# Performance work log

Measured on AMD Instinct MI355X. Metric: run time of the kernel, lower is better.

Reference implementation:

```python
import jax, jax.numpy as jnp
import numpy as np

NUM_HEADS = 8

def _ln(x, w, b, eps=1e-5):
    m = x.mean(-1, keepdims=True)
    v = ((x - m) ** 2).mean(-1, keepdims=True)
    return (x - m) / jnp.sqrt(v + eps) * w + b

def _conv3(x, w, b):
    y = jax.lax.conv_general_dilated(x, w, (1, 1), 'SAME',
                                     dimension_numbers=('NCHW', 'OIHW', 'NCHW'))
    return y + b[None, :, None, None]

def _pos_encoding(c, h, w, dtype):
    # first c//2 channels: x position in [0,1]; next c//2: y position
    px = jnp.broadcast_to(jnp.linspace(0, 1, w, dtype=dtype)[None, :], (h, w))
    py = jnp.broadcast_to(jnp.linspace(0, 1, h, dtype=dtype)[:, None], (h, w))
    pe = jnp.concatenate([jnp.broadcast_to(px, (c // 2, h, w)),
                          jnp.broadcast_to(py, (c // 2, h, w))], axis=0)
    return pe[None]  # [1,c,h,w]

def _pixel_shuffle(x, r=2):
    b, c4, h, w = x.shape
    c = c4 // (r * r)
    return x.reshape(b, c, r, r, h, w).transpose(0, 1, 4, 2, 5, 3).reshape(b, c, h * r, w * r)

def _forward(x, text_hidden, proj_w, proj_b, cf_w, cf_b,
             blk_qw, blk_qb, blk_kw, blk_kb, blk_vw, blk_vb,
             blk_ow, blk_ob, blk_ln1w, blk_ln1b, blk_ln2w, blk_ln2b,
             up_w, up_b, cl_w, cl_b):
    B = x.shape[0]
    # text projection: [B, L, text_dim] -> [B, L, C]
    tf = jnp.einsum('bld,cd->blc', text_hidden, proj_w) + proj_b
    feat = _conv3(x, cf_w, cf_b)  # [B, C, H, W]
    _, C, H, W = feat.shape
    L = tf.shape[1]
    hd = C // NUM_HEADS
    scale = hd ** (-0.5)
    pe = _pos_encoding(C, H, W, feat.dtype)

    def block(feat, p):
        qw, qb, kw, kb, vw, vb, ow, ob, l1w, l1b, l2w, l2b = p
        q = jnp.einsum('oi,bihw->bohw', qw, feat) + qb[None, :, None, None]
        q = q + pe * 0.05
        q_flat = q.reshape(B, C, H * W).transpose(0, 2, 1)  # [B, HW, C]
        q_norm = _ln(q_flat, l1w, l1b)
        qh = q_norm.reshape(B, H * W, NUM_HEADS, hd).transpose(0, 2, 1, 3)
        k = jnp.einsum('blc,oc->blo', tf, kw) + kb
        v = jnp.einsum('blc,oc->blo', tf, vw) + vb
        kn = _ln(k, l2w, l2b)
        kh = kn.reshape(B, L, NUM_HEADS, hd).transpose(0, 2, 1, 3)
        vh = v.reshape(B, L, NUM_HEADS, hd).transpose(0, 2, 1, 3)
        attn = jax.nn.softmax(jnp.einsum('bhnd,bhld->bhnl', qh, kh) * scale, axis=-1)
        out = jnp.einsum('bhnl,bhld->bhnd', attn, vh)          # [B, H8, HW, hd]
        out = out.transpose(0, 2, 1, 3).reshape(B, H * W, C)   # [B, HW, C]
        out = out.transpose(0, 2, 1).reshape(B, C, H, W)
        out = jnp.einsum('oi,bihw->bohw', ow, out) + ob[None, :, None, None]
        return out + feat, None

    blk_params = (blk_qw, blk_qb, blk_kw, blk_kb, blk_vw, blk_vb,
                  blk_ow, blk_ob, blk_ln1w, blk_ln1b, blk_ln2w, blk_ln2b)
    feat, _ = jax.lax.scan(block, feat, blk_params)

    for i in range(up_w.shape[0]):
        feat = jax.nn.relu(_pixel_shuffle(_conv3(feat, up_w[i], up_b[i]), 2))
    return _conv3(feat, cl_w, cl_b)


def setup_inputs() -> dict:
    key = jax.random.key(0)
    ks = jax.random.split(key, 20)
    B, H, W = 8, 64, 64
    C, D, L, NB = 64, 512, 77, 16
    s = 0.05
    inp = {
        'x': jax.random.normal(ks[0], (B, 3, H, W), jnp.float32),
        'text_hidden': jax.random.normal(ks[1], (B, L, D), jnp.float32),
        'proj_w': jax.random.normal(ks[2], (C, D), jnp.float32) * 0.01,
        'proj_b': jnp.zeros((C,), jnp.float32),
        'cf_w': jax.random.normal(ks[3], (C, 3, 3, 3), jnp.float32) * s,
        'cf_b': jnp.zeros((C,), jnp.float32),
        'blk_qw': jax.random.normal(ks[4], (NB, C, C), jnp.float32) * s,
        'blk_qb': jnp.zeros((NB, C), jnp.float32),
        'blk_kw': jax.random.normal(ks[5], (NB, C, C), jnp.float32) * 0.01,
        'blk_kb': jnp.zeros((NB, C), jnp.float32),
        'blk_vw': jax.random.normal(ks[6], (NB, C, C), jnp.float32) * 0.01,
        'blk_vb': jnp.zeros((NB, C), jnp.float32),
        'blk_ow': jax.random.normal(ks[7], (NB, C, C), jnp.float32) * s,
        'blk_ob': jnp.zeros((NB, C), jnp.float32),
        'blk_ln1w': jnp.ones((NB, C), jnp.float32),
        'blk_ln1b': jnp.zeros((NB, C), jnp.float32),
        'blk_ln2w': jnp.ones((NB, C), jnp.float32),
        'blk_ln2b': jnp.zeros((NB, C), jnp.float32),
        'up_w': jax.random.normal(ks[8], (2, C * 4, C, 3, 3), jnp.float32) * s,
        'up_b': jnp.zeros((2, C * 4), jnp.float32),
        'cl_w': jax.random.normal(ks[9], (3, C, 3, 3), jnp.float32) * s,
        'cl_b': jnp.zeros((3,), jnp.float32),
    }
    return inp


def reference(x, text_hidden, proj_w, proj_b, cf_w, cf_b,
              blk_qw, blk_qb, blk_kw, blk_kb, blk_vw, blk_vb,
              blk_ow, blk_ob, blk_ln1w, blk_ln1b, blk_ln2w, blk_ln2b,
              up_w, up_b, cl_w, cl_b):
    return _forward(x, text_hidden, proj_w, proj_b, cf_w, cf_b,
                    blk_qw, blk_qb, blk_kw, blk_kb, blk_vw, blk_vb,
                    blk_ow, blk_ob, blk_ln1w, blk_ln1b, blk_ln2w, blk_ln2b,
                    up_w, up_b, cl_w, cl_b)
```

## Files before the change

### kernel.cpp

```cpp
#include <hip/hip_runtime.h>
#include <math.h>

#define BATCH 8
#define C 64
#define NH 8
#define HD 8
#define LTXT 77
#define H0 64
#define W0 64
#define HW0 (H0*W0)

typedef __attribute__((ext_vector_type(8))) short bfrag;
typedef __attribute__((ext_vector_type(4))) float ffrag;
typedef __attribute__((ext_vector_type(8))) unsigned short us8;
typedef __attribute__((ext_vector_type(4))) unsigned short us4;
typedef __attribute__((ext_vector_type(2))) float f2;

__device__ __forceinline__ unsigned short f2bf(float f) {
    unsigned u = __builtin_bit_cast(unsigned, f);
    u += 0x7fff + ((u >> 16) & 1);
    return (unsigned short)(u >> 16);
}

__global__ void text_proj_kernel(const float* __restrict__ th, const float* __restrict__ pw,
                                 const float* __restrict__ pb, float* __restrict__ tf) {
    __shared__ float sh[512];
    int bl = blockIdx.x;
    int c = threadIdx.x;
    const float* row = th + (size_t)bl * 512;
    for (int i = c; i < 512; i += 64) sh[i] = row[i];
    __syncthreads();
    const float* wrow = pw + c * 512;
    float acc = pb[c];
    for (int i = 0; i < 512; i += 4) {
        acc += sh[i] * wrow[i] + sh[i+1] * wrow[i+1] + sh[i+2] * wrow[i+2] + sh[i+3] * wrow[i+3];
    }
    tf[bl * 64 + c] = acc;
}

__global__ void __launch_bounds__(256)
prep_kernel(const float* __restrict__ x, const float* __restrict__ cf_w,
            const float* __restrict__ cf_b, float* __restrict__ feat,
            const float* __restrict__ up_w,
            unsigned short* __restrict__ PW1, unsigned short* __restrict__ PW2,
            const float* __restrict__ cl_w, unsigned short* __restrict__ PWF,
            const float* __restrict__ qw, const float* __restrict__ ow,
            unsigned short* __restrict__ PQ, unsigned short* __restrict__ PO) {
    int blk = blockIdx.x;
    if (blk < 8192) {
        int idx = blk * 256 + threadIdx.x;
        int wx = idx & 63;
        int h = (idx >> 6) & 63;
        int o = (idx >> 12) & 63;
        int b = idx >> 18;
        const float* wr = cf_w + o * 27;
        float acc = cf_b[o];
        for (int ci = 0; ci < 3; ci++) {
            for (int ky = 0; ky < 3; ky++) {
                int y = h + ky - 1;
                if ((unsigned)y >= 64u) continue;
                const float* xr = x + (((size_t)b * 3 + ci) * 64 + y) * 64;
                const float* wk = wr + ci * 9 + ky * 3;
                if (wx > 0) acc += xr[wx - 1] * wk[0];
                acc += xr[wx] * wk[1];
                if (wx < 63) acc += xr[wx + 1] * wk[2];
            }
        }
        feat[idx] = acc;
    } else if (blk < 8192 + 1152) {
        int e0 = blk - 8192;
        int st = e0 / 576;
        int e = (e0 % 576) * 256 + threadIdx.x;
        const float* w = up_w + (size_t)st * 147456;
        unsigned short* d = st ? PW2 : PW1;
        int j = e & 7, n = (e >> 3) & 255, q = (e >> 11) & 3, s = (e >> 13) & 1, t = e >> 14;
        int c = n & 63, g = n >> 6;
        int co = 4 * c + g, ci = 32 * s + 8 * q + j;
        d[e] = f2bf(w[co * 576 + ci * 9 + t]);
    } else if (blk < 8192 + 1152 + 36) {
        int e = (blk - 8192 - 1152) * 256 + threadIdx.x;
        int j = e & 7, n = (e >> 3) & 15, q = (e >> 7) & 3, s = (e >> 9) & 1, t = e >> 10;
        int ci = 32 * s + 8 * q + j;
        float v = (n < 3) ? cl_w[n * 576 + ci * 9 + t] : 0.f;
        PWF[e] = f2bf(v);
    } else {
        int e = (blk - 8192 - 1152 - 36) * 256 + threadIdx.x;
        int j = e & 7, n = (e >> 3) & 63, quad = (e >> 9) & 3, kt = (e >> 11) & 1, layer = e >> 12;
        int c = kt * 32 + quad * 8 + j;
        PQ[e] = f2bf(qw[layer * 4096 + n * 64 + c]);
        PO[e] = f2bf(ow[layer * 4096 + n * 64 + c]);
    }
}

__global__ void kv_all_kernel(const float* __restrict__ tf,
                              const float* __restrict__ kw, const float* __restrict__ kb,
                              const float* __restrict__ vw, const float* __restrict__ vb,
                              const float* __restrict__ l2w, const float* __restrict__ l2b,
                              float* __restrict__ kbuf, float* __restrict__ vbuf) {
    __shared__ float sh[64];
    int g = blockIdx.x;
    int bl = g % (BATCH * LTXT);
    int blk = g / (BATCH * LTXT);
    int o = threadIdx.x;
    sh[o] = tf[bl * 64 + o];
    __syncthreads();
    const float* kr = kw + blk * 4096 + o * 64;
    const float* vr = vw + blk * 4096 + o * 64;
    float ka = kb[blk * 64 + o], va = vb[blk * 64 + o];
    for (int c2 = 0; c2 < 64; c2++) {
        float t = sh[c2];
        ka += t * kr[c2];
        va += t * vr[c2];
    }
    float s = ka;
    for (int off = 32; off; off >>= 1) s += __shfl_xor(s, off, 64);
    float mean = s * (1.0f / 64.0f);
    float d = ka - mean;
    float s2 = d * d;
    for (int off = 32; off; off >>= 1) s2 += __shfl_xor(s2, off, 64);
    float rstd = rsqrtf(s2 * (1.0f / 64.0f) + 1e-5f);
    size_t outi = (size_t)blk * (BATCH * LTXT * 64) + (size_t)bl * 64 + o;
    kbuf[outi] = (d * rstd * l2w[blk * 64 + o] + l2b[blk * 64 + o]) * 0.51006973f;
    vbuf[outi] = va;
}

__global__ void __launch_bounds__(1024, 8)
attn_all_kernel(const float* __restrict__ feat,
                const float* __restrict__ kbuf, const float* __restrict__ vbuf,
                const unsigned short* __restrict__ PQ, const unsigned short* __restrict__ PO,
                const float* __restrict__ qb_a, const float* __restrict__ ob_a,
                const float* __restrict__ l1w_a, const float* __restrict__ l1b_a,
                unsigned short* __restrict__ X1) {
    __shared__ __attribute__((aligned(16))) unsigned short sfb[64][72];
    __shared__ __attribute__((aligned(16))) unsigned short sob[64][72];
    __shared__ __attribute__((aligned(16))) float qf[64][68];
    __shared__ float so[64][64];
    __shared__ __attribute__((aligned(16))) float red[2][4][64];
    __shared__ float ss1[8][64];

    int b = blockIdx.x >> 6;
    int tile = blockIdx.x & 63;
    int n0 = tile << 6;
    int wv = __builtin_amdgcn_readfirstlane(threadIdx.x >> 6);
    int lane = threadIdx.x & 63;
    int p = lane;
    int quad = lane >> 4, n16 = lane & 15;
    int mt = wv >> 2, nt = wv & 3;
    int o0 = wv * 4;
    int h = wv >> 1, half = wv & 1;
    int a0 = h * 8;
    const float* fbase = feat + ((size_t)b << 18) + n0;

    float rres[4];
#pragma unroll
    for (int j = 0; j < 4; j++) rres[j] = fbase[(o0 + j) * HW0 + p];
    {
        us4 v;
#pragma unroll
        for (int j = 0; j < 4; j++) v[j] = f2bf(rres[j]);
        *(us4*)&sfb[p][o0] = v;
    }

    const float pxk = 0.05f / 63.0f;
    float py005 = (float)tile * pxk;
    __syncthreads();

#pragma unroll 1
    for (int layer = 0; layer < 16; layer++) {
        const float* qb = qb_a + layer * 64;
        const float* ob = ob_a + layer * 64;
        const float* l1w = l1w_a + layer * 64;
        const float* l1b = l1b_a + layer * 64;

        {
            bfrag af0 = *(const bfrag*)&sfb[mt * 16 + n16][quad * 8];
            bfrag af1 = *(const bfrag*)&sfb[mt * 16 + n16][32 + quad * 8];
            const unsigned short* bq = PQ + layer * 4096 + (size_t)((quad * 64) + nt * 16 + n16) * 8;
            bfrag bf0 = *(const bfrag*)bq;
            bfrag bf1 = *(const bfrag*)(bq + 2048);
            ffrag cc = (ffrag)0.f;
            cc = __builtin_amdgcn_mfma_f32_16x16x32_bf16(af0, bf0, cc, 0, 0, 0);
            cc = __builtin_amdgcn_mfma_f32_16x16x32_bf16(af1, bf1, cc, 0, 0, 0);
            int cch = nt * 16 + n16;
            float qbv = qb[cch];
            int p0 = mt * 16 + quad * 4;
            float pe0 = (nt < 2) ? (float)p0 * pxk : py005;
            float ped = (nt < 2) ? pxk : 0.f;
            float ov[4];
            ov[0] = cc[0] + qbv + pe0;
            ov[1] = cc[1] + qbv + pe0 + ped;
            ov[2] = cc[2] + qbv + pe0 + 2.f * ped;
            ov[3] = cc[3] + qbv + pe0 + 3.f * ped;
            float4 o4 = {ov[0], ov[1], ov[2], ov[3]};
            *(float4*)&qf[cch][p0] = o4;

            float sv[4], sq[4];
#pragma unroll
            for (int r = 0; r < 4; r++) {
                float s = ov[r], s2v = ov[r] * ov[r];
                s += __shfl_xor(s, 1);  s2v += __shfl_xor(s2v, 1);
                s += __shfl_xor(s, 2);  s2v += __shfl_xor(s2v, 2);
                s += __shfl_xor(s, 4);  s2v += __shfl_xor(s2v, 4);
                s += __shfl_xor(s, 8);  s2v += __shfl_xor(s2v, 8);
                sv[r] = s; sq[r] = s2v;
            }
            if (n16 == 0) {
                *(float4*)&red[0][nt][p0] = (float4){sv[0], sv[1], sv[2], sv[3]};
                *(float4*)&red[1][nt][p0] = (float4){sq[0], sq[1], sq[2], sq[3]};
            }
        }
        __syncthreads();

        {
            float ts = red[0][0][p] + red[0][1][p] + red[0][2][p] + red[0][3][p];
            float ts2 = red[1][0][p] + red[1][1][p] + red[1][2][p] + red[1][3][p];
            float mean = ts * (1.0f / 64.0f);
            float var = ts2 * (1.0f / 64.0f) - mean * mean;
            float rstd = rsqrtf(var + 1e-5f);

            f2 qv[4];
#pragma unroll
            for (int j = 0; j < 4; j++) {
                float qa  = (qf[a0 + 2 * j][p]     - mean) * rstd * l1w[a0 + 2 * j]     + l1b[a0 + 2 * j];
                float qbv = (qf[a0 + 2 * j + 1][p] - mean) * rstd * l1w[a0 + 2 * j + 1] + l1b[a0 + 2 * j + 1];
                qv[j][0] = qa;
                qv[j][1] = qbv;
            }
            const float* kb_b = kbuf + ((size_t)layer * BATCH * LTXT + (size_t)b * LTXT) * 64 + a0;
            const float* vb_b = vbuf + ((size_t)layer * BATCH * LTXT + (size_t)b * LTXT) * 64 + a0;
            int l0 = half ? 39 : 0;
            int l1 = half ? 77 : 39;
            float ssum = 0.f;
            f2 acc2[4] = {(f2)0.f, (f2)0.f, (f2)0.f, (f2)0.f};
            for (int l = l0; l < l1; l++) {
                const float4* kr = (const float4*)(kb_b + l * 64);
                float4 k0 = kr[0], k1 = kr[1];
                f2 d2 = qv[0] * (f2){k0.x, k0.y};
                d2 += qv[1] * (f2){k0.z, k0.w};
                d2 += qv[2] * (f2){k1.x, k1.y};
                d2 += qv[3] * (f2){k1.z, k1.w};
                float e = exp2f(d2[0] + d2[1]);
                ssum += e;
                const float4* vr = (const float4*)(vb_b + l * 64);
                float4 v0 = vr[0], v1 = vr[1];
                f2 e2 = {e, e};
                acc2[0] += e2 * (f2){v0.x, v0.y};
                acc2[1] += e2 * (f2){v0.z, v0.w};
                acc2[2] += e2 * (f2){v1.x, v1.y};
                acc2[3] += e2 * (f2){v1.z, v1.w};
            }
            if (half) {
#pragma unroll
                for (int j = 0; j < 4; j++) {
                    so[a0 + 2 * j][p] = acc2[j][0];
                    so[a0 + 2 * j + 1][p] = acc2[j][1];
                }
                ss1[h][p] = ssum;
            }
            __syncthreads();
            if (!half) {
                float inv = 1.0f / (ssum + ss1[h][p]);
                us8 v;
#pragma unroll
                for (int j = 0; j < 4; j++) {
                    v[2*j]   = f2bf((acc2[j][0] + so[a0 + 2*j][p]) * inv);
                    v[2*j+1] = f2bf((acc2[j][1] + so[a0 + 2*j+1][p]) * inv);
                }
                *(us8*)&sob[p][a0] = v;
            }
        }
        __syncthreads();

        {
            bfrag af0 = *(const bfrag*)&sob[mt * 16 + n16][quad * 8];
            bfrag af1 = *(const bfrag*)&sob[mt * 16 + n16][32 + quad * 8];
            const unsigned short* bo = PO + layer * 4096 + (size_t)((quad * 64) + nt * 16 + n16) * 8;
            bfrag bf0 = *(const bfrag*)bo;
            bfrag bf1 = *(const bfrag*)(bo + 2048);
            ffrag cc = (ffrag)0.f;
            cc = __builtin_amdgcn_mfma_f32_16x16x32_bf16(af0, bf0, cc, 0, 0, 0);
            cc = __builtin_amdgcn_mfma_f32_16x16x32_bf16(af1, bf1, cc, 0, 0, 0);
            int cch = nt * 16 + n16;
            float obv = ob[cch];
            int p0 = mt * 16 + quad * 4;
            float4 o4;
            o4.x = cc[0] + obv; o4.y = cc[1] + obv; o4.z = cc[2] + obv; o4.w = cc[3] + obv;
            *(float4*)&qf[cch][p0] = o4;
        }
        __syncthreads();

        {
            us4 v;
#pragma unroll
            for (int j = 0; j < 4; j++) {
                rres[j] += qf[o0 + j][p];
                v[j] = f2bf(rres[j]);
            }
            *(us4*)&sfb[p][o0] = v;
        }
        __syncthreads();
    }

    us4 v;
#pragma unroll
    for (int j = 0; j < 4; j++) v[j] = f2bf(rres[j]);
    *(us4*)(X1 + ((size_t)(b * 4096 + n0 + p)) * 64 + o0) = v;
}

__global__ void __launch_bounds__(256)
upconv_mfma_kernel(const unsigned short* __restrict__ X, const unsigned short* __restrict__ Bp,
                   const float* __restrict__ bias, unsigned short* __restrict__ Y,
                   int Hin, int Win) {
    __shared__ __attribute__((aligned(16))) unsigned short sx[3 * 66 * 72];

    int y = blockIdx.y;
    int wv = threadIdx.x >> 6;
    int lane = threadIdx.x & 63;
    int q = lane >> 4, n16 = lane & 15;
    int m0 = blockIdx.x * 64;
    int hw = Hin * Win;
    int b = m0 / hw, rem = m0 % hw;
    int h = rem / Win, w0 = rem % Win;
    const unsigned short* Xb = X + (size_t)b * hw * 64;

    const us8 z8 = (us8)(unsigned short)0;
    for (int e = threadIdx.x; e < 1584; e += 256) {
        int ch8 = e & 7;
        int pxi = (e >> 3) % 66;
        int row = e / 528;
        int hh = h + row - 1, wp = w0 + pxi - 1;
        us8 v = z8;
        if ((unsigned)hh < (unsigned)Hin && (unsigned)wp < (unsigned)Win)
            v = *(const us8*)(Xb + ((size_t)hh * Win + wp) * 64 + ch8 * 8);
        *(us8*)&sx[row * 4752 + pxi * 72 + ch8 * 8] = v;
    }
    __syncthreads();

    ffrag acc[4][2];
#pragma unroll
    for (int i = 0; i < 4; i++)
#pragma unroll
        for (int j2 = 0; j2 < 2; j2++) acc[i][j2] = (ffrag)0.f;

    int npb = y * 128 + wv * 32;

    for (int t = 0; t < 9; t++) {
        int dy = t / 3, dx = t % 3;
        bfrag af[4][2];
#pragma unroll
        for (int mt = 0; mt < 4; mt++) {
            const unsigned short* sp = &sx[dy * 4752 + (mt * 16 + n16 + dx) * 72 + q * 8];
            af[mt][0] = *(const bfrag*)sp;
            af[mt][1] = *(const bfrag*)(sp + 32);
        }
#pragma unroll
        for (int s = 0; s < 2; s++) {
#pragma unroll
            for (int nt = 0; nt < 2; nt++) {
                bfrag bf = *(const bfrag*)(Bp + (size_t)((((t * 2 + s) * 4 + q) * 256) + npb + nt * 16 + n16) * 8);
#pragma unroll
                for (int mt = 0; mt < 4; mt++)
                    acc[mt][nt] = __builtin_amdgcn_mfma_f32_16x16x32_bf16(af[mt][s], bf, acc[mt][nt], 0, 0, 0);
            }
        }
    }

    int g = y * 2 + (wv >> 1);
    int r1 = y, r2 = wv >> 1;
    int cbase = (wv & 1) * 32;
    float bv[2];
#pragma unroll
    for (int nt = 0; nt < 2; nt++) bv[nt] = bias[4 * (cbase + nt * 16 + n16) + g];
    int Wo = Win * 2;
    unsigned short* Yb = Y + ((size_t)b * Hin * 2 * Wo + (size_t)(2 * h + r1) * Wo + r2) * 64;
#pragma unroll
    for (int mt = 0; mt < 4; mt++) {
#pragma unroll
        for (int r = 0; r < 4; r++) {
            int m = mt * 16 + q * 4 + r;
            unsigned short* dst = Yb + (size_t)(2 * (w0 + m)) * 64;
#pragma unroll
            for (int nt = 0; nt < 2; nt++) {
                float v = acc[mt][nt][r] + bv[nt];
                v = fmaxf(v, 0.f);
                dst[cbase + nt * 16 + n16] = f2bf(v);
            }
        }
    }
}

__global__ void __launch_bounds__(256)
final_mfma_kernel(const unsigned short* __restrict__ X, const unsigned short* __restrict__ Bp,
                  const float* __restrict__ bias, float* __restrict__ out) {
    __shared__ __attribute__((aligned(16))) unsigned short sx[6 * 66 * 72];

    int t0 = blockIdx.x;
    int wseg = t0 & 3;
    int rg = (t0 >> 2) & 63;
    int b = t0 >> 8;
    int y0 = rg * 4, w0 = wseg * 64;
    int wv = threadIdx.x >> 6, lane = threadIdx.x & 63;
    int q = lane >> 4, n16 = lane & 15;
    const unsigned short* Xb = X + (size_t)b * 65536 * 64;

    const us8 z8 = (us8)(unsigned short)0;
    for (int e = threadIdx.x; e < 3168; e += 256) {
        int ch8 = e & 7;
        int pxi = (e >> 3) % 66;
        int row = e / 528;
        int hh = y0 - 1 + row, wp = w0 - 1 + pxi;
        us8 v = z8;
        if ((unsigned)hh < 256u && (unsigned)wp < 256u)
            v = *(const us8*)(Xb + ((size_t)hh * 256 + wp) * 64 + ch8 * 8);
        *(us8*)&sx[row * 4752 + pxi * 72 + ch8 * 8] = v;
    }
    __syncthreads();

    ffrag acc[4];
#pragma unroll
    for (int i = 0; i < 4; i++) acc[i] = (ffrag)0.f;

    for (int t = 0; t < 9; t++) {
        int dy = t / 3, dx = t % 3;
        bfrag af[4][2];
#pragma unroll
        for (int mt = 0; mt < 4; mt++) {
            const unsigned short* sp = &sx[(wv + dy) * 4752 + (mt * 16 + n16 + dx) * 72 + q * 8];
            af[mt][0] = *(const bfrag*)sp;
            af[mt][1] = *(const bfrag*)(sp + 32);
        }
#pragma unroll
        for (int s = 0; s < 2; s++) {
            bfrag bf = *(const bfrag*)(Bp + (size_t)((((t * 2 + s) * 4 + q) * 16) + n16) * 8);
#pragma unroll
            for (int mt = 0; mt < 4; mt++)
                acc[mt] = __builtin_amdgcn_mfma_f32_16x16x32_bf16(af[mt][s], bf, acc[mt], 0, 0, 0);
        }
    }

    if (n16 < 3) {
        float bj = bias[n16];
        float* ob = out + (((size_t)b * 3 + n16) * 256 + (y0 + wv)) * 256;
#pragma unroll
        for (int mt = 0; mt < 4; mt++)
#pragma unroll
            for (int r = 0; r < 4; r++)
                ob[w0 + mt * 16 + q * 4 + r] = acc[mt][r] + bj;
    }
}

extern "C" void kernel_launch(void* const* d_in, const int* in_sizes, int n_in,
                              void* d_out, int out_size, void* d_ws, size_t ws_size,
                              hipStream_t stream) {
    const float* x      = (const float*)d_in[0];
    const float* th     = (const float*)d_in[1];
    const float* proj_w = (const float*)d_in[2];
    const float* proj_b = (const float*)d_in[3];
    const float* cf_w   = (const float*)d_in[4];
    const float* cf_b   = (const float*)d_in[5];
    const float* qw     = (const float*)d_in[6];
    const float* qb     = (const float*)d_in[7];
    const float* kw     = (const float*)d_in[8];
    const float* kb     = (const float*)d_in[9];
    const float* vw     = (const float*)d_in[10];
    const float* vb     = (const float*)d_in[11];
    const float* ow     = (const float*)d_in[12];
    const float* ob     = (const float*)d_in[13];
    const float* l1w    = (const float*)d_in[14];
    const float* l1b    = (const float*)d_in[15];
    const float* l2w    = (const float*)d_in[16];
    const float* l2b    = (const float*)d_in[17];
    const float* up_w   = (const float*)d_in[18];
    const float* up_b   = (const float*)d_in[19];
    const float* cl_w   = (const float*)d_in[20];
    const float* cl_b   = (const float*)d_in[21];

    float* ws   = (float*)d_ws;
    float* feat = ws;
    float* tf   = feat + 2097152;
    float* kbuf = tf + 39424;
    float* vbuf = kbuf + 630784;
    unsigned short* X1  = (unsigned short*)(vbuf + 630784);
    unsigned short* X2  = X1 + 2097152;
    unsigned short* X3  = X2 + 8388608;
    unsigned short* PW1 = X3 + 33554432;
    unsigned short* PW2 = PW1 + 147456;
    unsigned short* PWF = PW2 + 147456;
    unsigned short* PQ  = PWF + 9216;
    unsigned short* PO  = PQ + 65536;

    hipLaunchKernelGGL(prep_kernel, dim3(8192 + 1152 + 36 + 256), dim3(256), 0, stream,
                       x, cf_w, cf_b, feat, up_w, PW1, PW2, cl_w, PWF, qw, ow, PQ, PO);
    hipLaunchKernelGGL(text_proj_kernel, dim3(BATCH * LTXT), dim3(64), 0, stream,
                       th, proj_w, proj_b, tf);
    hipLaunchKernelGGL(kv_all_kernel, dim3(16 * BATCH * LTXT), dim3(64), 0, stream,
                       tf, kw, kb, vw, vb, l2w, l2b, kbuf, vbuf);

    hipLaunchKernelGGL(attn_all_kernel, dim3(BATCH * (HW0 / 64)), dim3(1024), 0, stream,
                       feat, kbuf, vbuf, PQ, PO, qb, ob, l1w, l1b, X1);

    hipLaunchKernelGGL(upconv_mfma_kernel, dim3(BATCH * 64 * 64 / 64, 2), dim3(256), 0, stream,
                       X1, PW1, up_b, X2, 64, 64);
    hipLaunchKernelGGL(upconv_mfma_kernel, dim3(BATCH * 128 * 128 / 64, 2), dim3(256), 0, stream,
                       X2, PW2, up_b + 256, X3, 128, 128);
    hipLaunchKernelGGL(final_mfma_kernel, dim3(BATCH * 64 * 4), dim3(256), 0, stream,
                       X3, PWF, cl_b, (float*)d_out);
}
```

Measured before the change: 583.1 us.

## Compute cross-attention scores and PV with bf16 MFMA instead of scalar FP32 loops

Moves the per-pixel attention over the 77 text tokens from scalar FP32 dot products to bf16 MFMA instructions, for both QK^T and P·V. The K/V producer now writes bf16 K padded to 80 rows and a transposed, padded V for MFMA-friendly loads. Q is normalized straight into a bf16 LDS tile, and the exp probabilities are staged in LDS as bf16, reusing a shared pool with qf. This trades FP32 accuracy in scores and probabilities for bf16, and adds four passes per layer, each with its own barriers, plus lanes that sit idle on padded MFMA tiles.

```diff
diff --git a/kernel.cpp b/kernel.cpp
--- a/kernel.cpp
+++ b/kernel.cpp
@@ -14,7 +14,6 @@
 typedef __attribute__((ext_vector_type(4))) float ffrag;
 typedef __attribute__((ext_vector_type(8))) unsigned short us8;
 typedef __attribute__((ext_vector_type(4))) unsigned short us4;
-typedef __attribute__((ext_vector_type(2))) float f2;
 
 __device__ __forceinline__ unsigned short f2bf(float f) {
     unsigned u = __builtin_bit_cast(unsigned, f);
@@ -96,21 +95,28 @@
                               const float* __restrict__ kw, const float* __restrict__ kb,
                               const float* __restrict__ vw, const float* __restrict__ vb,
                               const float* __restrict__ l2w, const float* __restrict__ l2b,
-                              float* __restrict__ kbuf, float* __restrict__ vbuf) {
+                              unsigned short* __restrict__ k16, unsigned short* __restrict__ vt16) {
     __shared__ float sh[64];
     int g = blockIdx.x;
-    int bl = g % (BATCH * LTXT);
-    int blk = g / (BATCH * LTXT);
+    int t = g % 96;
+    int lb = g / 96;
+    int b = lb & 7;
+    int blk = lb >> 3;
     int o = threadIdx.x;
-    sh[o] = tf[bl * 64 + o];
+    if (t >= LTXT) {
+        if (t < 80) k16[((size_t)lb * 80 + t) * 64 + o] = 0;
+        vt16[((size_t)lb * 64 + o) * 96 + t] = 0;
+        return;
+    }
+    sh[o] = tf[(b * LTXT + t) * 64 + o];
     __syncthreads();
-    const float* kr = kw + blk * 4096 + o * 64;
-    const float* vr = vw + blk * 4096 + o * 64;
+    const float* krw = kw + blk * 4096 + o * 64;
+    const float* vrw = vw + blk * 4096 + o * 64;
     float ka = kb[blk * 64 + o], va = vb[blk * 64 + o];
     for (int c2 = 0; c2 < 64; c2++) {
-        float t = sh[c2];
-        ka += t * kr[c2];
-        va += t * vr[c2];
+        float tv = sh[c2];
+        ka += tv * krw[c2];
+        va += tv * vrw[c2];
     }
     float s = ka;
     for (int off = 32; off; off >>= 1) s += __shfl_xor(s, off, 64);
@@ -119,24 +125,27 @@
     float s2 = d * d;
     for (int off = 32; off; off >>= 1) s2 += __shfl_xor(s2, off, 64);
     float rstd = rsqrtf(s2 * (1.0f / 64.0f) + 1e-5f);
-    size_t outi = (size_t)blk * (BATCH * LTXT * 64) + (size_t)bl * 64 + o;
-    kbuf[outi] = (d * rstd * l2w[blk * 64 + o] + l2b[blk * 64 + o]) * 0.51006973f;
-    vbuf[outi] = va;
+    float kn = (d * rstd * l2w[blk * 64 + o] + l2b[blk * 64 + o]) * 0.51006973f;
+    k16[((size_t)lb * 80 + t) * 64 + o] = f2bf(kn);
+    vt16[((size_t)lb * 64 + o) * 96 + t] = f2bf(va);
 }
 
 __global__ void __launch_bounds__(1024, 8)
 attn_all_kernel(const float* __restrict__ feat,
-                const float* __restrict__ kbuf, const float* __restrict__ vbuf,
+                const unsigned short* __restrict__ k16, const unsigned short* __restrict__ vt16,
                 const unsigned short* __restrict__ PQ, const unsigned short* __restrict__ PO,
                 const float* __restrict__ qb_a, const float* __restrict__ ob_a,
                 const float* __restrict__ l1w_a, const float* __restrict__ l1b_a,
                 unsigned short* __restrict__ X1) {
     __shared__ __attribute__((aligned(16))) unsigned short sfb[64][72];
     __shared__ __attribute__((aligned(16))) unsigned short sob[64][72];
-    __shared__ __attribute__((aligned(16))) float qf[64][68];
-    __shared__ float so[64][64];
+    __shared__ __attribute__((aligned(16))) unsigned short qn[64][72];
     __shared__ __attribute__((aligned(16))) float red[2][4][64];
-    __shared__ float ss1[8][64];
+    __shared__ float dpart[2][8][16];
+    __shared__ __attribute__((aligned(16))) char upool[2 * 64 * 104 * 2];
+
+    unsigned short (*P16)[64][104] = (unsigned short (*)[64][104])upool;
+    float (*qf)[68] = (float (*)[68])upool;
 
     int b = blockIdx.x >> 6;
     int tile = blockIdx.x & 63;
@@ -147,8 +156,10 @@
     int quad = lane >> 4, n16 = lane & 15;
     int mt = wv >> 2, nt = wv & 3;
     int o0 = wv * 4;
-    int h = wv >> 1, half = wv & 1;
-    int a0 = h * 8;
+    int cch = nt * 16 + n16;
+    int p0 = mt * 16 + quad * 4;
+    int h1 = wv >> 3, ntp = (wv >> 1) & 3, ms = wv & 1;
+    int pxl = ntp * 16 + n16;
     const float* fbase = feat + ((size_t)b << 18) + n0;
 
     float rres[4];
@@ -163,6 +174,7 @@
 
     const float pxk = 0.05f / 63.0f;
     float py005 = (float)tile * pxk;
+    const bfrag zb = (bfrag)(short)0;
     __syncthreads();
 
 #pragma unroll 1
@@ -171,28 +183,25 @@
         const float* ob = ob_a + layer * 64;
         const float* l1w = l1w_a + layer * 64;
         const float* l1b = l1b_a + layer * 64;
-
+        size_t kvbase = (size_t)layer * BATCH + b;
+
+        float ov[4];
         {
             bfrag af0 = *(const bfrag*)&sfb[mt * 16 + n16][quad * 8];
             bfrag af1 = *(const bfrag*)&sfb[mt * 16 + n16][32 + quad * 8];
-            const unsigned short* bq = PQ + layer * 4096 + (size_t)((quad * 64) + nt * 16 + n16) * 8;
-            bfrag bf0 = *(const bfrag*)bq;
-            bfrag bf1 = *(const bfrag*)(bq + 2048);
+            const unsigned short* bqp = PQ + layer * 4096 + (size_t)((quad * 64) + nt * 16 + n16) * 8;
+            bfrag bf0 = *(const bfrag*)bqp;
+            bfrag bf1 = *(const bfrag*)(bqp + 2048);
             ffrag cc = (ffrag)0.f;
             cc = __builtin_amdgcn_mfma_f32_16x16x32_bf16(af0, bf0, cc, 0, 0, 0);
             cc = __builtin_amdgcn_mfma_f32_16x16x32_bf16(af1, bf1, cc, 0, 0, 0);
-            int cch = nt * 16 + n16;
             float qbv = qb[cch];
-            int p0 = mt * 16 + quad * 4;
             float pe0 = (nt < 2) ? (float)p0 * pxk : py005;
             float ped = (nt < 2) ? pxk : 0.f;
-            float ov[4];
             ov[0] = cc[0] + qbv + pe0;
             ov[1] = cc[1] + qbv + pe0 + ped;
             ov[2] = cc[2] + qbv + pe0 + 2.f * ped;
             ov[3] = cc[3] + qbv + pe0 + 3.f * ped;
-            float4 o4 = {ov[0], ov[1], ov[2], ov[3]};
-            *(float4*)&qf[cch][p0] = o4;
 
             float sv[4], sq[4];
 #pragma unroll
@@ -212,64 +221,84 @@
         __syncthreads();
 
         {
-            float ts = red[0][0][p] + red[0][1][p] + red[0][2][p] + red[0][3][p];
-            float ts2 = red[1][0][p] + red[1][1][p] + red[1][2][p] + red[1][3][p];
-            float mean = ts * (1.0f / 64.0f);
-            float var = ts2 * (1.0f / 64.0f) - mean * mean;
-            float rstd = rsqrtf(var + 1e-5f);
-
-            f2 qv[4];
-#pragma unroll
-            for (int j = 0; j < 4; j++) {
-                float qa  = (qf[a0 + 2 * j][p]     - mean) * rstd * l1w[a0 + 2 * j]     + l1b[a0 + 2 * j];
-                float qbv = (qf[a0 + 2 * j + 1][p] - mean) * rstd * l1w[a0 + 2 * j + 1] + l1b[a0 + 2 * j + 1];
-                qv[j][0] = qa;
-                qv[j][1] = qbv;
-            }
-            const float* kb_b = kbuf + ((size_t)layer * BATCH * LTXT + (size_t)b * LTXT) * 64 + a0;
-            const float* vb_b = vbuf + ((size_t)layer * BATCH * LTXT + (size_t)b * LTXT) * 64 + a0;
-            int l0 = half ? 39 : 0;
-            int l1 = half ? 77 : 39;
-            float ssum = 0.f;
-            f2 acc2[4] = {(f2)0.f, (f2)0.f, (f2)0.f, (f2)0.f};
-            for (int l = l0; l < l1; l++) {
-                const float4* kr = (const float4*)(kb_b + l * 64);
-                float4 k0 = kr[0], k1 = kr[1];
-                f2 d2 = qv[0] * (f2){k0.x, k0.y};
-                d2 += qv[1] * (f2){k0.z, k0.w};
-                d2 += qv[2] * (f2){k1.x, k1.y};
-                d2 += qv[3] * (f2){k1.z, k1.w};
-                float e = exp2f(d2[0] + d2[1]);
-                ssum += e;
-                const float4* vr = (const float4*)(vb_b + l * 64);
-                float4 v0 = vr[0], v1 = vr[1];
-                f2 e2 = {e, e};
-                acc2[0] += e2 * (f2){v0.x, v0.y};
-                acc2[1] += e2 * (f2){v0.z, v0.w};
-                acc2[2] += e2 * (f2){v1.x, v1.y};
-                acc2[3] += e2 * (f2){v1.z, v1.w};
-            }
-            if (half) {
-#pragma unroll
-                for (int j = 0; j < 4; j++) {
-                    so[a0 + 2 * j][p] = acc2[j][0];
-                    so[a0 + 2 * j + 1][p] = acc2[j][1];
+            ffrag ts = (ffrag)0.f, tq = (ffrag)0.f;
+#pragma unroll
+            for (int g4 = 0; g4 < 4; g4++) {
+                ts += *(const ffrag*)&red[0][g4][p0];
+                tq += *(const ffrag*)&red[1][g4][p0];
+            }
+            float wch = l1w[cch], bch = l1b[cch];
+#pragma unroll
+            for (int r = 0; r < 4; r++) {
+                float mean = ts[r] * (1.0f / 64.0f);
+                float var = tq[r] * (1.0f / 64.0f) - mean * mean;
+                float rstd = rsqrtf(var + 1e-5f);
+                qn[p0 + r][cch] = f2bf((ov[r] - mean) * rstd * wch + bch);
+            }
+        }
+        __syncthreads();
+
+#pragma unroll 1
+        for (int pass = 0; pass < 4; pass++) {
+            int h = pass * 2 + h1;
+            {
+                bfrag bq = zb;
+                if (quad == 0) bq = *(const bfrag*)&qn[pxl][h * 8];
+                const unsigned short* kr = k16 + kvbase * (80 * 64) + h * 8;
+                float dsum = 0.f;
+
+#define S_MT(mtc) { \
+    bfrag ak = zb; \
+    if (quad == 0) ak = *(const bfrag*)(kr + ((mtc) * 16 + n16) * 64); \
+    ffrag cc = (ffrag)0.f; \
+    cc = __builtin_amdgcn_mfma_f32_16x16x32_bf16(ak, bq, cc, 0, 0, 0); \
+    float e0 = exp2f(cc[0]), e1 = exp2f(cc[1]), e2 = exp2f(cc[2]), e3 = exp2f(cc[3]); \
+    if ((mtc) == 4) { \
+        int tb = 64 + quad * 4; \
+        if (tb + 0 >= 77) e0 = 0.f; \
+        if (tb + 1 >= 77) e1 = 0.f; \
+        if (tb + 2 >= 77) e2 = 0.f; \
+        if (tb + 3 >= 77) e3 = 0.f; \
+    } \
+    dsum += (e0 + e1) + (e2 + e3); \
+    unsigned long long pw = (unsigned long long)((unsigned)f2bf(e0) | ((unsigned)f2bf(e1) << 16)) \
+                          | ((unsigned long long)((unsigned)f2bf(e2) | ((unsigned)f2bf(e3) << 16)) << 32); \
+    *(unsigned long long*)&P16[h1][pxl][(mtc) * 16 + quad * 4] = pw; \
+}
+                if (ms == 0) {
+                    S_MT(0); S_MT(1); S_MT(2);
+                } else {
+                    S_MT(3); S_MT(4);
+                    *(unsigned long long*)&P16[h1][pxl][80 + quad * 4] = 0ull;
                 }
-                ss1[h][p] = ssum;
+#undef S_MT
+                dsum += __shfl_xor(dsum, 16, 64);
+                dsum += __shfl_xor(dsum, 32, 64);
+                if (quad == 0) dpart[ms][h1 * 4 + ntp][n16] = dsum;
             }
             __syncthreads();
-            if (!half) {
-                float inv = 1.0f / (ssum + ss1[h][p]);
-                us8 v;
-#pragma unroll
-                for (int j = 0; j < 4; j++) {
-                    v[2*j]   = f2bf((acc2[j][0] + so[a0 + 2*j][p]) * inv);
-                    v[2*j+1] = f2bf((acc2[j][1] + so[a0 + 2*j+1][p]) * inv);
+
+            if (ms == 0) {
+                float den = dpart[0][h1 * 4 + ntp][n16] + dpart[1][h1 * 4 + ntp][n16];
+                float inv = 1.0f / den;
+                const unsigned short* vr = vt16 + (kvbase * 64 + h * 8 + n16) * 96;
+                ffrag acc = (ffrag)0.f;
+#pragma unroll
+                for (int kk = 0; kk < 3; kk++) {
+                    bfrag av = zb;
+                    if (n16 < 8) av = *(const bfrag*)(vr + kk * 32 + quad * 8);
+                    bfrag bp = *(const bfrag*)&P16[h1][pxl][kk * 32 + quad * 8];
+                    acc = __builtin_amdgcn_mfma_f32_16x16x32_bf16(av, bp, acc, 0, 0, 0);
                 }
-                *(us8*)&sob[p][a0] = v;
-            }
-        }
-        __syncthreads();
+                if (quad < 2) {
+                    us4 v4;
+#pragma unroll
+                    for (int r = 0; r < 4; r++) v4[r] = f2bf(acc[r] * inv);
+                    *(us4*)&sob[pxl][h * 8 + quad * 4] = v4;
+                }
+            }
+            __syncthreads();
+        }
 
         {
             bfrag af0 = *(const bfrag*)&sob[mt * 16 + n16][quad * 8];
@@ -280,9 +309,7 @@
             ffrag cc = (ffrag)0.f;
             cc = __builtin_amdgcn_mfma_f32_16x16x32_bf16(af0, bf0, cc, 0, 0, 0);
             cc = __builtin_amdgcn_mfma_f32_16x16x32_bf16(af1, bf1, cc, 0, 0, 0);
-            int cch = nt * 16 + n16;
             float obv = ob[cch];
-            int p0 = mt * 16 + quad * 4;
             float4 o4;
             o4.x = cc[0] + obv; o4.y = cc[1] + obv; o4.z = cc[2] + obv; o4.w = cc[3] + obv;
             *(float4*)&qf[cch][p0] = o4;
@@ -478,9 +505,9 @@
     float* ws   = (float*)d_ws;
     float* feat = ws;
     float* tf   = feat + 2097152;
-    float* kbuf = tf + 39424;
-    float* vbuf = kbuf + 630784;
-    unsigned short* X1  = (unsigned short*)(vbuf + 630784);
+    unsigned short* k16 = (unsigned short*)(tf + 39424);
+    unsigned short* vt16 = k16 + 655360;
+    unsigned short* X1  = vt16 + 786432;
     unsigned short* X2  = X1 + 2097152;
     unsigned short* X3  = X2 + 8388608;
     unsigned short* PW1 = X3 + 33554432;
@@ -493,11 +520,11 @@
                        x, cf_w, cf_b, feat, up_w, PW1, PW2, cl_w, PWF, qw, ow, PQ, PO);
     hipLaunchKernelGGL(text_proj_kernel, dim3(BATCH * LTXT), dim3(64), 0, stream,
                        th, proj_w, proj_b, tf);
-    hipLaunchKernelGGL(kv_all_kernel, dim3(16 * BATCH * LTXT), dim3(64), 0, stream,
-                       tf, kw, kb, vw, vb, l2w, l2b, kbuf, vbuf);
+    hipLaunchKernelGGL(kv_all_kernel, dim3(16 * BATCH * 96), dim3(64), 0, stream,
+                       tf, kw, kb, vw, vb, l2w, l2b, k16, vt16);
 
     hipLaunchKernelGGL(attn_all_kernel, dim3(BATCH * (HW0 / 64)), dim3(1024), 0, stream,
-                       feat, kbuf, vbuf, PQ, PO, qb, ob, l1w, l1b, X1);
+                       feat, k16, vt16, PQ, PO, qb, ob, l1w, l1b, X1);
 
     hipLaunchKernelGGL(upconv_mfma_kernel, dim3(BATCH * 64 * 64 / 64, 2), dim3(256), 0, stream,
                        X1, PW1, up_b, X2, 64, 64);
```

Result: slower. 602.0 us (+3.2%).
